# Kernel tuning notes

Hardware: AMD Instinct MI355X
Metric: run time of the kernel (lower is better)

Reference implementation:

```python
import jax, jax.numpy as jnp
import numpy as np

B, T, D = 4096, 200, 64
NEG_INF = -(2.0 ** 32) + 1.0  # matches tf paddings constant


def setup_inputs() -> dict:
    key = jax.random.key(0)
    ks = jax.random.split(key, 12)
    queries = jax.random.normal(ks[0], (B, D), dtype=jnp.float32)
    keys = jax.random.normal(ks[1], (B, T, D), dtype=jnp.float32)
    keys_length = jax.random.randint(ks[2], (B,), 0, 200, dtype=jnp.int32)
    # attention MLP params (glorot-ish scale)
    W1 = jax.random.normal(ks[3], (4 * D, 16), dtype=jnp.float32) * (1.0 / np.sqrt(4 * D))
    b1 = jnp.zeros((16,), dtype=jnp.float32)
    W2 = jax.random.normal(ks[4], (16, 8), dtype=jnp.float32) * (1.0 / np.sqrt(16))
    b2 = jnp.zeros((8,), dtype=jnp.float32)
    W3 = jax.random.normal(ks[5], (8, 1), dtype=jnp.float32) * (1.0 / np.sqrt(8))
    b3 = jnp.zeros((1,), dtype=jnp.float32)
    W4 = jax.random.normal(ks[6], (D, D), dtype=jnp.float32) * (1.0 / np.sqrt(D))
    b4 = jnp.zeros((D,), dtype=jnp.float32)
    return {"queries": queries, "keys": keys, "keys_length": keys_length,
            "W1": W1, "b1": b1, "W2": W2, "b2": b2, "W3": W3, "b3": b3,
            "W4": W4, "b4": b4}


def reference(queries, keys, keys_length, W1, b1, W2, b2, W3, b3, W4, b4):
    Bq, Tq, Dq = keys.shape
    # tile queries across time: [B, T, D]
    q = jnp.broadcast_to(queries[:, None, :], (Bq, Tq, Dq))
    # DIN feature construction: [B, T, 4D]
    din_all = jnp.concatenate([q, keys, q - keys, q * keys], axis=-1)
    # tiny MLP scorer
    x = jax.nn.sigmoid(jnp.einsum('btf,fh->bth', din_all, W1) + b1)
    x = jax.nn.sigmoid(jnp.einsum('bth,hk->btk', x, W2) + b2)
    scores = (jnp.einsum('btk,ko->bto', x, W3) + b3)[..., 0]  # [B, T]
    # mask invalid history positions
    mask = jnp.arange(Tq, dtype=keys_length.dtype)[None, :] < keys_length[:, None]
    scores = jnp.where(mask, scores, NEG_INF)
    scores = scores / (Dq ** 0.5)  # scaling applied after masking, as in tf code
    attn = jax.nn.softmax(scores, axis=-1)  # [B, T]
    out = jnp.einsum('bt,btd->bd', attn, keys)  # weighted sum of keys
    out = out @ W4 + b4  # [B, D]
    return out
```

## Files before the change

### kernel.cpp

```cpp
#include <hip/hip_runtime.h>
#include <math.h>

#define TT 200
#define DD 64
#define MTS 72

typedef __attribute__((ext_vector_type(8))) short bf16x8;
typedef __attribute__((ext_vector_type(4))) float f32x4;

__device__ __forceinline__ float sigmoidf_(float x) {
    return 1.0f / (1.0f + __expf(-x));
}
__device__ __forceinline__ short f2bf(float x) {
    unsigned u = __float_as_uint(x);
    u += 0x7fff + ((u >> 16) & 1);
    return (short)(u >> 16);
}
__device__ __forceinline__ float bf2f(short s) {
    return __uint_as_float(((unsigned)(unsigned short)s) << 16);
}
__device__ __forceinline__ void build_hi(float4 v0, float4 v1, bf16x8& hi) {
    float xs[8] = {v0.x, v0.y, v0.z, v0.w, v1.x, v1.y, v1.z, v1.w};
    #pragma unroll
    for (int j = 0; j < 8; j++) hi[j] = f2bf(xs[j]);
}

__global__ __launch_bounds__(256) void din_attn_kernel(
    const float* __restrict__ queries,
    const float* __restrict__ keys,
    const int*   __restrict__ keys_length,
    const float* __restrict__ W1,
    const float* __restrict__ b1,
    const float* __restrict__ W2,
    const float* __restrict__ b2,
    const float* __restrict__ W3,
    const float* __restrict__ b3,
    const float* __restrict__ W4,
    const float* __restrict__ b4,
    float* __restrict__ out)
{
    __shared__ __align__(16) short MtHi[16 * MTS];
    __shared__ __align__(16) short MtLo[16 * MTS];
    __shared__ __align__(16) short H1s[208 * 16];
    __shared__ float cred[4 * 16];
    __shared__ __align__(16) float w2s[16 * 8];
    __shared__ float w3s[8];
    __shared__ float b2s[8];
    __shared__ float b3sh[1];
    __shared__ float scoresS[256];
    __shared__ float sred[8];
    __shared__ float wred[4 * 64];
    __shared__ float tmpv[64];

    const int tid  = threadIdx.x;
    const int b    = blockIdx.x;
    const int w    = tid >> 6;
    const int lane = tid & 63;
    const int m16  = lane & 15;
    const int quad = lane >> 4;
    const int len  = keys_length[b];
    const float* kb = keys + (size_t)b * (TT * DD);

    int trow0 = w * 16 + m16;
    if (trow0 > TT - 1) trow0 = TT - 1;
    const float* kp0 = kb + trow0 * 64 + quad * 8;
    float4 c0 = *(const float4*)(kp0);
    float4 c1 = *(const float4*)(kp0 + 4);
    float4 c2 = *(const float4*)(kp0 + 32);
    float4 c3 = *(const float4*)(kp0 + 36);

    {
        const int d  = tid >> 2;
        const int hg = tid & 3;
        const float q = queries[b * 64 + d];
        const float4* W1v = (const float4*)W1;
        float4 a  = W1v[(0   + d) * 4 + hg];
        float4 bb = W1v[(64  + d) * 4 + hg];
        float4 cc = W1v[(128 + d) * 4 + hg];
        float4 dd = W1v[(192 + d) * 4 + hg];
        float cp[4], mv[4];
        cp[0] = q * (a.x + cc.x);  mv[0] = bb.x - cc.x + q * dd.x;
        cp[1] = q * (a.y + cc.y);  mv[1] = bb.y - cc.y + q * dd.y;
        cp[2] = q * (a.z + cc.z);  mv[2] = bb.z - cc.z + q * dd.z;
        cp[3] = q * (a.w + cc.w);  mv[3] = bb.w - cc.w + q * dd.w;
        #pragma unroll
        for (int i = 0; i < 4; i++) {
            const int h = hg * 4 + i;
            short hi = f2bf(mv[i]);
            MtHi[h * MTS + d] = hi;
            MtLo[h * MTS + d] = f2bf(mv[i] - bf2f(hi));
        }
        #pragma unroll
        for (int mask = 4; mask <= 32; mask <<= 1) {
            #pragma unroll
            for (int i = 0; i < 4; i++) cp[i] += __shfl_xor(cp[i], mask, 64);
        }
        if (lane < 4) {
            #pragma unroll
            for (int i = 0; i < 4; i++) cred[w * 16 + lane * 4 + i] = cp[i];
        }
        if (tid < 128)       w2s[tid]        = W2[tid];
        else if (tid < 136)  w3s[tid - 128]  = W3[tid - 128];
        else if (tid < 144)  b2s[tid - 136]  = b2[tid - 136];
        else if (tid == 144) b3sh[0]         = b3[0];
    }
    __syncthreads();

    {
        const int bb0 = m16 * MTS + quad * 8;
        bf16x8 Bh0 = *(const bf16x8*)&MtHi[bb0];
        bf16x8 Bh1 = *(const bf16x8*)&MtHi[bb0 + 32];
        bf16x8 Bl0 = *(const bf16x8*)&MtLo[bb0];
        bf16x8 Bl1 = *(const bf16x8*)&MtLo[bb0 + 32];
        const float cv = b1[m16] + cred[0 + m16] + cred[16 + m16]
                       + cred[32 + m16] + cred[48 + m16];

        for (int tile = w; tile < 13; tile += 4) {
            float4 n0, n1, n2, n3;
            const int nt = tile + 4;
            if (nt < 13) {
                int trow = nt * 16 + m16;
                if (trow > TT - 1) trow = TT - 1;
                const float* kp = kb + trow * 64 + quad * 8;
                n0 = *(const float4*)(kp);
                n1 = *(const float4*)(kp + 4);
                n2 = *(const float4*)(kp + 32);
                n3 = *(const float4*)(kp + 36);
            }
            bf16x8 ah0, ah1;
            build_hi(c0, c1, ah0);
            build_hi(c2, c3, ah1);
            f32x4 acc = {0.f, 0.f, 0.f, 0.f};
            acc = __builtin_amdgcn_mfma_f32_16x16x32_bf16(ah0, Bh0, acc, 0, 0, 0);
            acc = __builtin_amdgcn_mfma_f32_16x16x32_bf16(ah0, Bl0, acc, 0, 0, 0);
            acc = __builtin_amdgcn_mfma_f32_16x16x32_bf16(ah1, Bh1, acc, 0, 0, 0);
            acc = __builtin_amdgcn_mfma_f32_16x16x32_bf16(ah1, Bl1, acc, 0, 0, 0);
            const int rb = tile * 16 + quad * 4;
            H1s[(rb + 0) * 16 + m16] = f2bf(sigmoidf_(acc[0] + cv));
            H1s[(rb + 1) * 16 + m16] = f2bf(sigmoidf_(acc[1] + cv));
            H1s[(rb + 2) * 16 + m16] = f2bf(sigmoidf_(acc[2] + cv));
            H1s[(rb + 3) * 16 + m16] = f2bf(sigmoidf_(acc[3] + cv));
            c0 = n0; c1 = n1; c2 = n2; c3 = n3;
        }
    }
    __syncthreads();

    float w4r[16];
    {
        const float* w4p = W4 + (size_t)(w * 16) * 64 + lane;
        #pragma unroll
        for (int i = 0; i < 16; i++) w4r[i] = w4p[i * 64];
    }
    float b4v = (tid < 64) ? b4[tid] : 0.0f;

    float sc = -INFINITY;
    if (tid < TT) {
        bf16x8 h1a = *(const bf16x8*)&H1s[tid * 16];
        bf16x8 h1b = *(const bf16x8*)&H1s[tid * 16 + 8];
        float hv[16];
        #pragma unroll
        for (int j = 0; j < 8; j++) { hv[j] = bf2f(h1a[j]); hv[8 + j] = bf2f(h1b[j]); }
        float s2[8];
        #pragma unroll
        for (int k = 0; k < 8; k++) s2[k] = b2s[k];
        #pragma unroll
        for (int h = 0; h < 16; h++) {
            const float hh = hv[h];
            const float4* w2r = (const float4*)&w2s[h * 8];
            float4 wa = w2r[0], wb = w2r[1];
            s2[0] = fmaf(hh, wa.x, s2[0]);
            s2[1] = fmaf(hh, wa.y, s2[1]);
            s2[2] = fmaf(hh, wa.z, s2[2]);
            s2[3] = fmaf(hh, wa.w, s2[3]);
            s2[4] = fmaf(hh, wb.x, s2[4]);
            s2[5] = fmaf(hh, wb.y, s2[5]);
            s2[6] = fmaf(hh, wb.z, s2[6]);
            s2[7] = fmaf(hh, wb.w, s2[7]);
        }
        float s3 = b3sh[0];
        #pragma unroll
        for (int k = 0; k < 8; k++) s3 = fmaf(sigmoidf_(s2[k]), w3s[k], s3);
        if (tid >= len) s3 = -4294967295.0f;
        sc = s3 * 0.125f;
    }

    float m = sc;
    #pragma unroll
    for (int off = 32; off >= 1; off >>= 1) m = fmaxf(m, __shfl_xor(m, off, 64));
    if (lane == 0) sred[w] = m;
    __syncthreads();
    m = fmaxf(fmaxf(sred[0], sred[1]), fmaxf(sred[2], sred[3]));

    float p = (tid < TT) ? __expf(sc - m) : 0.0f;
    scoresS[tid] = p;
    float ssum = p;
    #pragma unroll
    for (int off = 32; off >= 1; off >>= 1) ssum += __shfl_xor(ssum, off, 64);
    if (lane == 0) sred[4 + w] = ssum;
    __syncthreads();

    float ws = 0.0f;
    #pragma unroll 10
    for (int t = w * 50; t < w * 50 + 50; t++)
        ws = fmaf(scoresS[t], kb[t * 64 + lane], ws);
    wred[w * 64 + lane] = ws;
    __syncthreads();
    if (tid < 64) {
        const float inv = 1.0f / (sred[4] + sred[5] + sred[6] + sred[7]);
        tmpv[tid] = (wred[tid] + wred[64 + tid] + wred[128 + tid] + wred[192 + tid]) * inv;
    }
    __syncthreads();

    float po = 0.0f;
    #pragma unroll
    for (int i = 0; i < 16; i++) po = fmaf(tmpv[w * 16 + i], w4r[i], po);
    wred[w * 64 + lane] = po;
    __syncthreads();
    if (tid < 64)
        out[(size_t)b * 64 + tid] =
            b4v + wred[tid] + wred[64 + tid] + wred[128 + tid] + wred[192 + tid];
}

extern "C" void kernel_launch(void* const* d_in, const int* in_sizes, int n_in,
                              void* d_out, int out_size, void* d_ws, size_t ws_size,
                              hipStream_t stream) {
    const float* queries     = (const float*)d_in[0];
    const float* keys        = (const float*)d_in[1];
    const int*   keys_length = (const int*)  d_in[2];
    const float* W1 = (const float*)d_in[3];
    const float* b1 = (const float*)d_in[4];
    const float* W2 = (const float*)d_in[5];
    const float* b2 = (const float*)d_in[6];
    const float* W3 = (const float*)d_in[7];
    const float* b3 = (const float*)d_in[8];
    const float* W4 = (const float*)d_in[9];
    const float* b4 = (const float*)d_in[10];
    float* out = (float*)d_out;

    const int Bn = in_sizes[2];
    din_attn_kernel<<<Bn, 256, 0, stream>>>(
        queries, keys, keys_length, W1, b1, W2, b2, W3, b3, W4, b4, out);
}
```

Before: 316.2 us.

## Assign one batch row per wavefront and remove block-level syncs

```diff
diff --git a/kernel.cpp b/kernel.cpp
--- a/kernel.cpp
+++ b/kernel.cpp
@@ -3,7 +3,7 @@
 
 #define TT 200
 #define DD 64
-#define MTS 72
+#define H1STR 20
 
 typedef __attribute__((ext_vector_type(8))) short bf16x8;
 typedef __attribute__((ext_vector_type(4))) float f32x4;
@@ -39,134 +39,130 @@
     const float* __restrict__ b4,
     float* __restrict__ out)
 {
-    __shared__ __align__(16) short MtHi[16 * MTS];
-    __shared__ __align__(16) short MtLo[16 * MTS];
-    __shared__ __align__(16) short H1s[208 * 16];
-    __shared__ float cred[4 * 16];
-    __shared__ __align__(16) float w2s[16 * 8];
-    __shared__ float w3s[8];
-    __shared__ float b2s[8];
-    __shared__ float b3sh[1];
-    __shared__ float scoresS[256];
-    __shared__ float sred[8];
-    __shared__ float wred[4 * 64];
-    __shared__ float tmpv[64];
+    __shared__ __align__(16) short H1s[4][208 * H1STR];
+    __shared__ __align__(16) float scoresS[4][200];
+    __shared__ __align__(16) float tmpv[4][64];
 
     const int tid  = threadIdx.x;
-    const int b    = blockIdx.x;
     const int w    = tid >> 6;
     const int lane = tid & 63;
     const int m16  = lane & 15;
     const int quad = lane >> 4;
+    const int b    = blockIdx.x * 4 + w;
     const int len  = keys_length[b];
     const float* kb = keys + (size_t)b * (TT * DD);
 
-    int trow0 = w * 16 + m16;
-    if (trow0 > TT - 1) trow0 = TT - 1;
-    const float* kp0 = kb + trow0 * 64 + quad * 8;
+    short* h1p = &H1s[w][0];
+    float* scp = &scoresS[w][0];
+    float* tvp = &tmpv[w][0];
+
+    const float* kp0 = kb + m16 * 64 + quad * 8;
     float4 c0 = *(const float4*)(kp0);
     float4 c1 = *(const float4*)(kp0 + 4);
     float4 c2 = *(const float4*)(kp0 + 32);
     float4 c3 = *(const float4*)(kp0 + 36);
 
+    bf16x8 Bh0, Bl0, Bh1, Bl1;
+    float cvec;
     {
-        const int d  = tid >> 2;
-        const int hg = tid & 3;
-        const float q = queries[b * 64 + d];
-        const float4* W1v = (const float4*)W1;
-        float4 a  = W1v[(0   + d) * 4 + hg];
-        float4 bb = W1v[(64  + d) * 4 + hg];
-        float4 cc = W1v[(128 + d) * 4 + hg];
-        float4 dd = W1v[(192 + d) * 4 + hg];
-        float cp[4], mv[4];
-        cp[0] = q * (a.x + cc.x);  mv[0] = bb.x - cc.x + q * dd.x;
-        cp[1] = q * (a.y + cc.y);  mv[1] = bb.y - cc.y + q * dd.y;
-        cp[2] = q * (a.z + cc.z);  mv[2] = bb.z - cc.z + q * dd.z;
-        cp[3] = q * (a.w + cc.w);  mv[3] = bb.w - cc.w + q * dd.w;
-        #pragma unroll
-        for (int i = 0; i < 4; i++) {
-            const int h = hg * 4 + i;
-            short hi = f2bf(mv[i]);
-            MtHi[h * MTS + d] = hi;
-            MtLo[h * MTS + d] = f2bf(mv[i] - bf2f(hi));
+        const int d0 = quad * 8;
+        const float* qb = queries + b * 64 + d0;
+        float4 qv0 = *(const float4*)(qb);
+        float4 qv1 = *(const float4*)(qb + 4);
+        float4 qv2 = *(const float4*)(qb + 32);
+        float4 qv3 = *(const float4*)(qb + 36);
+        float qa[8] = {qv0.x, qv0.y, qv0.z, qv0.w, qv1.x, qv1.y, qv1.z, qv1.w};
+        float qc[8] = {qv2.x, qv2.y, qv2.z, qv2.w, qv3.x, qv3.y, qv3.z, qv3.w};
+        float cp = 0.0f;
+        #pragma unroll
+        for (int j = 0; j < 8; j++) {
+            {
+                const int d = d0 + j;
+                float a  = W1[(0   + d) * 16 + m16];
+                float bb = W1[(64  + d) * 16 + m16];
+                float cc = W1[(128 + d) * 16 + m16];
+                float dd = W1[(192 + d) * 16 + m16];
+                float mv = bb - cc + qa[j] * dd;
+                cp = fmaf(qa[j], a + cc, cp);
+                short hi = f2bf(mv);
+                Bh0[j] = hi;
+                Bl0[j] = f2bf(mv - bf2f(hi));
+            }
+            {
+                const int d = d0 + j + 32;
+                float a  = W1[(0   + d) * 16 + m16];
+                float bb = W1[(64  + d) * 16 + m16];
+                float cc = W1[(128 + d) * 16 + m16];
+                float dd = W1[(192 + d) * 16 + m16];
+                float mv = bb - cc + qc[j] * dd;
+                cp = fmaf(qc[j], a + cc, cp);
+                short hi = f2bf(mv);
+                Bh1[j] = hi;
+                Bl1[j] = f2bf(mv - bf2f(hi));
+            }
         }
-        #pragma unroll
-        for (int mask = 4; mask <= 32; mask <<= 1) {
-            #pragma unroll
-            for (int i = 0; i < 4; i++) cp[i] += __shfl_xor(cp[i], mask, 64);
+        cp += __shfl_xor(cp, 16, 64);
+        cp += __shfl_xor(cp, 32, 64);
+        cvec = b1[m16] + cp;
+    }
+
+    #pragma unroll 1
+    for (int tile = 0; tile < 13; tile++) {
+        float4 n0, n1, n2, n3;
+        if (tile < 12) {
+            int trow = (tile + 1) * 16 + m16;
+            if (trow > TT - 1) trow = TT - 1;
+            const float* kp = kb + trow * 64 + quad * 8;
+            n0 = *(const float4*)(kp);
+            n1 = *(const float4*)(kp + 4);
+            n2 = *(const float4*)(kp + 32);
+            n3 = *(const float4*)(kp + 36);
         }
-        if (lane < 4) {
-            #pragma unroll
-            for (int i = 0; i < 4; i++) cred[w * 16 + lane * 4 + i] = cp[i];
-        }
-        if (tid < 128)       w2s[tid]        = W2[tid];
-        else if (tid < 136)  w3s[tid - 128]  = W3[tid - 128];
-        else if (tid < 144)  b2s[tid - 136]  = b2[tid - 136];
-        else if (tid == 144) b3sh[0]         = b3[0];
-    }
-    __syncthreads();
-
-    {
-        const int bb0 = m16 * MTS + quad * 8;
-        bf16x8 Bh0 = *(const bf16x8*)&MtHi[bb0];
-        bf16x8 Bh1 = *(const bf16x8*)&MtHi[bb0 + 32];
-        bf16x8 Bl0 = *(const bf16x8*)&MtLo[bb0];
-        bf16x8 Bl1 = *(const bf16x8*)&MtLo[bb0 + 32];
-        const float cv = b1[m16] + cred[0 + m16] + cred[16 + m16]
-                       + cred[32 + m16] + cred[48 + m16];
-
-        for (int tile = w; tile < 13; tile += 4) {
-            float4 n0, n1, n2, n3;
-            const int nt = tile + 4;
-            if (nt < 13) {
-                int trow = nt * 16 + m16;
-                if (trow > TT - 1) trow = TT - 1;
-                const float* kp = kb + trow * 64 + quad * 8;
-                n0 = *(const float4*)(kp);
-                n1 = *(const float4*)(kp + 4);
-                n2 = *(const float4*)(kp + 32);
-                n3 = *(const float4*)(kp + 36);
-            }
-            bf16x8 ah0, ah1;
-            build_hi(c0, c1, ah0);
-            build_hi(c2, c3, ah1);
-            f32x4 acc = {0.f, 0.f, 0.f, 0.f};
-            acc = __builtin_amdgcn_mfma_f32_16x16x32_bf16(ah0, Bh0, acc, 0, 0, 0);
-            acc = __builtin_amdgcn_mfma_f32_16x16x32_bf16(ah0, Bl0, acc, 0, 0, 0);
-            acc = __builtin_amdgcn_mfma_f32_16x16x32_bf16(ah1, Bh1, acc, 0, 0, 0);
-            acc = __builtin_amdgcn_mfma_f32_16x16x32_bf16(ah1, Bl1, acc, 0, 0, 0);
-            const int rb = tile * 16 + quad * 4;
-            H1s[(rb + 0) * 16 + m16] = f2bf(sigmoidf_(acc[0] + cv));
-            H1s[(rb + 1) * 16 + m16] = f2bf(sigmoidf_(acc[1] + cv));
-            H1s[(rb + 2) * 16 + m16] = f2bf(sigmoidf_(acc[2] + cv));
-            H1s[(rb + 3) * 16 + m16] = f2bf(sigmoidf_(acc[3] + cv));
-            c0 = n0; c1 = n1; c2 = n2; c3 = n3;
-        }
-    }
-    __syncthreads();
-
-    float w4r[16];
-    {
-        const float* w4p = W4 + (size_t)(w * 16) * 64 + lane;
-        #pragma unroll
-        for (int i = 0; i < 16; i++) w4r[i] = w4p[i * 64];
-    }
-    float b4v = (tid < 64) ? b4[tid] : 0.0f;
-
-    float sc = -INFINITY;
-    if (tid < TT) {
-        bf16x8 h1a = *(const bf16x8*)&H1s[tid * 16];
-        bf16x8 h1b = *(const bf16x8*)&H1s[tid * 16 + 8];
+        bf16x8 ah0, ah1;
+        build_hi(c0, c1, ah0);
+        build_hi(c2, c3, ah1);
+        f32x4 acc = {0.f, 0.f, 0.f, 0.f};
+        acc = __builtin_amdgcn_mfma_f32_16x16x32_bf16(ah0, Bh0, acc, 0, 0, 0);
+        acc = __builtin_amdgcn_mfma_f32_16x16x32_bf16(ah0, Bl0, acc, 0, 0, 0);
+        acc = __builtin_amdgcn_mfma_f32_16x16x32_bf16(ah1, Bh1, acc, 0, 0, 0);
+        acc = __builtin_amdgcn_mfma_f32_16x16x32_bf16(ah1, Bl1, acc, 0, 0, 0);
+        const int rb = tile * 16 + quad * 4;
+        h1p[(rb + 0) * H1STR + m16] = f2bf(sigmoidf_(acc[0] + cvec));
+        h1p[(rb + 1) * H1STR + m16] = f2bf(sigmoidf_(acc[1] + cvec));
+        h1p[(rb + 2) * H1STR + m16] = f2bf(sigmoidf_(acc[2] + cvec));
+        h1p[(rb + 3) * H1STR + m16] = f2bf(sigmoidf_(acc[3] + cvec));
+        c0 = n0; c1 = n1; c2 = n2; c3 = n3;
+    }
+
+    float w3v[8], b2v[8];
+    #pragma unroll
+    for (int k = 0; k < 8; k++) { w3v[k] = W3[k]; b2v[k] = b2[k]; }
+    const float b3v = b3[0];
+
+    float sc[4];
+    #pragma unroll
+    for (int i = 0; i < 4; i++) {
+        int t  = lane + 64 * i;
+        int tr = (t > 207) ? 207 : t;
+        const uint2* hrow = (const uint2*)&h1p[tr * H1STR];
+        uint2 u0 = hrow[0], u1 = hrow[1], u2 = hrow[2], u3 = hrow[3];
         float hv[16];
-        #pragma unroll
-        for (int j = 0; j < 8; j++) { hv[j] = bf2f(h1a[j]); hv[8 + j] = bf2f(h1b[j]); }
+        hv[0]  = __uint_as_float(u0.x << 16); hv[1]  = __uint_as_float(u0.x & 0xffff0000u);
+        hv[2]  = __uint_as_float(u0.y << 16); hv[3]  = __uint_as_float(u0.y & 0xffff0000u);
+        hv[4]  = __uint_as_float(u1.x << 16); hv[5]  = __uint_as_float(u1.x & 0xffff0000u);
+        hv[6]  = __uint_as_float(u1.y << 16); hv[7]  = __uint_as_float(u1.y & 0xffff0000u);
+        hv[8]  = __uint_as_float(u2.x << 16); hv[9]  = __uint_as_float(u2.x & 0xffff0000u);
+        hv[10] = __uint_as_float(u2.y << 16); hv[11] = __uint_as_float(u2.y & 0xffff0000u);
+        hv[12] = __uint_as_float(u3.x << 16); hv[13] = __uint_as_float(u3.x & 0xffff0000u);
+        hv[14] = __uint_as_float(u3.y << 16); hv[15] = __uint_as_float(u3.y & 0xffff0000u);
+
         float s2[8];
         #pragma unroll
-        for (int k = 0; k < 8; k++) s2[k] = b2s[k];
+        for (int k = 0; k < 8; k++) s2[k] = b2v[k];
         #pragma unroll
         for (int h = 0; h < 16; h++) {
             const float hh = hv[h];
-            const float4* w2r = (const float4*)&w2s[h * 8];
+            const float4* w2r = (const float4*)&W2[h * 8];
             float4 wa = w2r[0], wb = w2r[1];
             s2[0] = fmaf(hh, wa.x, s2[0]);
             s2[1] = fmaf(hh, wa.y, s2[1]);
@@ -177,48 +173,58 @@
             s2[6] = fmaf(hh, wb.z, s2[6]);
             s2[7] = fmaf(hh, wb.w, s2[7]);
         }
-        float s3 = b3sh[0];
-        #pragma unroll
-        for (int k = 0; k < 8; k++) s3 = fmaf(sigmoidf_(s2[k]), w3s[k], s3);
-        if (tid >= len) s3 = -4294967295.0f;
-        sc = s3 * 0.125f;
-    }
-
-    float m = sc;
+        float s3 = b3v;
+        #pragma unroll
+        for (int k = 0; k < 8; k++) s3 = fmaf(sigmoidf_(s2[k]), w3v[k], s3);
+        if (t >= len) s3 = -4294967295.0f;
+        sc[i] = s3 * 0.125f;
+    }
+
+    float m = fmaxf(fmaxf(sc[0], sc[1]), fmaxf(sc[2], sc[3]));
     #pragma unroll
     for (int off = 32; off >= 1; off >>= 1) m = fmaxf(m, __shfl_xor(m, off, 64));
-    if (lane == 0) sred[w] = m;
-    __syncthreads();
-    m = fmaxf(fmaxf(sred[0], sred[1]), fmaxf(sred[2], sred[3]));
-
-    float p = (tid < TT) ? __expf(sc - m) : 0.0f;
-    scoresS[tid] = p;
-    float ssum = p;
+    float p[4];
+    float ssum = 0.0f;
+    #pragma unroll
+    for (int i = 0; i < 4; i++) {
+        int t = lane + 64 * i;
+        p[i] = (t < TT) ? __expf(sc[i] - m) : 0.0f;
+        ssum += p[i];
+    }
     #pragma unroll
     for (int off = 32; off >= 1; off >>= 1) ssum += __shfl_xor(ssum, off, 64);
-    if (lane == 0) sred[4 + w] = ssum;
-    __syncthreads();
+    const float inv = 1.0f / ssum;
+    #pragma unroll
+    for (int i = 0; i < 4; i++) {
+        int t = lane + 64 * i;
+        if (t < TT) scp[t] = p[i];
+    }
 
     float ws = 0.0f;
-    #pragma unroll 10
-    for (int t = w * 50; t < w * 50 + 50; t++)
-        ws = fmaf(scoresS[t], kb[t * 64 + lane], ws);
-    wred[w * 64 + lane] = ws;
-    __syncthreads();
-    if (tid < 64) {
-        const float inv = 1.0f / (sred[4] + sred[5] + sred[6] + sred[7]);
-        tmpv[tid] = (wred[tid] + wred[64 + tid] + wred[128 + tid] + wred[192 + tid]) * inv;
-    }
-    __syncthreads();
-
-    float po = 0.0f;
-    #pragma unroll
-    for (int i = 0; i < 16; i++) po = fmaf(tmpv[w * 16 + i], w4r[i], po);
-    wred[w * 64 + lane] = po;
-    __syncthreads();
-    if (tid < 64)
-        out[(size_t)b * 64 + tid] =
-            b4v + wred[tid] + wred[64 + tid] + wred[128 + tid] + wred[192 + tid];
+    const float4* sp4 = (const float4*)scp;
+    #pragma unroll 5
+    for (int g = 0; g < 50; g++) {
+        float4 pv = sp4[g];
+        const float* kq = kb + (g * 4) * 64 + lane;
+        ws = fmaf(pv.x, kq[0],   ws);
+        ws = fmaf(pv.y, kq[64],  ws);
+        ws = fmaf(pv.z, kq[128], ws);
+        ws = fmaf(pv.w, kq[192], ws);
+    }
+    tvp[lane] = ws * inv;
+
+    float o = b4[lane];
+    const float4* tv4 = (const float4*)tvp;
+    #pragma unroll 4
+    for (int g = 0; g < 16; g++) {
+        float4 tv = tv4[g];
+        const float* w4q = W4 + (g * 4) * 64 + lane;
+        o = fmaf(tv.x, w4q[0],   o);
+        o = fmaf(tv.y, w4q[64],  o);
+        o = fmaf(tv.z, w4q[128], o);
+        o = fmaf(tv.w, w4q[192], o);
+    }
+    out[(size_t)b * 64 + lane] = o;
 }
 
 extern "C" void kernel_launch(void* const* d_in, const int* in_sizes, int n_in,
@@ -238,6 +244,6 @@
     float* out = (float*)d_out;
 
     const int Bn = in_sizes[2];
-    din_attn_kernel<<<Bn, 256, 0, stream>>>(
+    din_attn_kernel<<<Bn / 4, 256, 0, stream>>>(
         queries, keys, keys_length, W1, b1, W2, b2, W3, b3, W4, b4, out);
 }
```

Measured after the change: 321.7 us. About the same (+1.8%).
